# Performance work log

Measured on AMD Instinct MI355X. Metric: run time of the kernel, lower is better.

## Reference

```python
import jax, jax.numpy as jnp
import numpy as np

COEF_DIM = 256  # must match init_kwargs coef_dim


def setup_inputs() -> dict:
    key = jax.random.key(0)
    k1, k2 = jax.random.split(key)
    # times in [0,1); with curr_t=1, t_scaled = 2*t - 1 lies in [-1,1)
    t = jax.random.uniform(k1, (4, 131072), dtype=jnp.float32)
    # learned HiPPO coefficients (buffer `coef` in the torch module)
    coef = jax.random.normal(k2, (COEF_DIM,), dtype=jnp.float32)
    return {"t": t, "coef": coef, "curr_t": 1}


def reference(t, coef, curr_t):
    """Signal reconstruction: sum_{i=1..N} coef[i-1]*sqrt(2i+1)*P_i(2t/curr_t-1).

    Instead of N independent legendre_polynomial_p calls (O(N^2) work),
    run the three-term Legendre recurrence once with lax.scan, fusing the
    coef-weighted accumulation into the carry (O(N) work per time point).
    """
    x = 2.0 * t / curr_t - 1.0            # scaled times, same shape as t
    n = coef.shape[0]
    i = jnp.arange(1, n + 1, dtype=jnp.float32)
    w = coef * jnp.sqrt(2.0 * i + 1.0)    # per-degree weight, degree i=1..N

    def step(carry, wi):
        pm1, p, acc = carry               # P_{deg-1}, P_deg, running sum
        w_next, deg = wi                  # weight for degree deg+1
        # P_{deg+1} = ((2*deg+1)*x*P_deg - deg*P_{deg-1}) / (deg+1)
        p_next = ((2.0 * deg + 1.0) * x * p - deg * pm1) / (deg + 1.0)
        return (p, p_next, acc + w_next * p_next), None

    # P_0 = 1, P_1 = x; accumulator starts with the degree-1 term w[0]*P_1
    init = (jnp.ones_like(x), x, w[0] * x)
    degs = jnp.arange(1, n, dtype=jnp.float32)
    (_, _, out), _ = jax.lax.scan(step, init, (w[1:], degs))
    return out
```

## Files before the change

### kernel.cpp

```cpp
#include <hip/hip_runtime.h>


#define NCOEF 256

__global__ __launch_bounds__(256) void hippo_kernel(
    const float* __restrict__ t,
    const float* __restrict__ coef,
    const int* __restrict__ curr_t,
    float* __restrict__ out,
    int n4)
{
    __shared__ float w[NCOEF];
    const int tid = threadIdx.x;
    w[tid] = coef[tid] * sqrtf(2.0f * (float)tid + 3.0f);
    __syncthreads();

    const int gid = blockIdx.x * 256 + tid;
    if (gid >= n4) return;

    const float s = 2.0f / (float)curr_t[0];

    float4 tv = reinterpret_cast<const float4*>(t)[gid];
    float x[4] = { tv.x * s - 1.0f, tv.y * s - 1.0f,
                   tv.z * s - 1.0f, tv.w * s - 1.0f };

    float pm1[4], p[4], acc[4];
    const float w0 = w[0];
#pragma unroll
    for (int e = 0; e < 4; ++e) {
        pm1[e] = 1.0f;
        p[e]   = x[e];
        acc[e] = w0 * x[e];
    }

#pragma unroll
    for (int d = 1; d < NCOEF; ++d) {
        const float a = (2.0f * (float)d + 1.0f) / ((float)d + 1.0f);
        const float b = (float)d / ((float)d + 1.0f);
        const float wd = w[d];
#pragma unroll
        for (int e = 0; e < 4; ++e) {
            float pn = a * (x[e] * p[e]) - b * pm1[e];
            pm1[e] = p[e];
            p[e]   = pn;
            acc[e] = fmaf(wd, pn, acc[e]);
        }
    }

    reinterpret_cast<float4*>(out)[gid] =
        make_float4(acc[0], acc[1], acc[2], acc[3]);
}

extern "C" void kernel_launch(void* const* d_in, const int* in_sizes, int n_in,
                              void* d_out, int out_size, void* d_ws, size_t ws_size,
                              hipStream_t stream)
{
    const float* t      = (const float*)d_in[0];
    const float* coef   = (const float*)d_in[1];
    const int*   curr_t = (const int*)d_in[2];
    float*       out    = (float*)d_out;

    int n  = in_sizes[0];
    int n4 = n >> 2;
    int blocks = (n4 + 255) / 256;
    hippo_kernel<<<blocks, 256, 0, stream>>>(t, coef, curr_t, out, n4);
}
```

Baseline: 67.23 us.

## Rescale Legendre recurrence to cut per-degree multiplies and pack coefficients in float4 table

Rewrites the Legendre three-term recurrence in a rescaled form, S = P/g with g computed via lgamma, so each step takes one multiply plus one fma instead of a multiply, multiply and fma. Precomputed per-degree constants and rescaled weights go into a shared float4 table, read two degrees per load. The loop is only partly unrolled now (unroll 2) instead of fully unrolled. The rescaling factors come from lgamma/exp, which may change numerical accuracy, and the setup cost per block rises because of the transcendental calls.

```diff
diff --git a/kernel.cpp b/kernel.cpp
--- a/kernel.cpp
+++ b/kernel.cpp
@@ -1,7 +1,20 @@
 #include <hip/hip_runtime.h>
+#include <math.h>
 
 
-#define NCOEF 256
+#define NPAIR 128
+
+__device__ inline float g_of(float fi) {
+    float lg = lgammaf(2.0f * fi) - (fi - 1.0f) * 1.3862943611f
+             - lgammaf(fi) - lgammaf(fi + 1.0f);
+    return expf(lg);
+}
+
+__device__ inline float wp_of(int i, const float* __restrict__ coef) {
+    if (i > 256) return 0.0f;
+    float fi = (float)i;
+    return coef[i - 1] * sqrtf(2.0f * fi + 1.0f) * g_of(fi);
+}
 
 __global__ __launch_bounds__(256) void hippo_kernel(
     const float* __restrict__ t,
@@ -10,9 +23,22 @@
     float* __restrict__ out,
     int n4)
 {
-    __shared__ float w[NCOEF];
+    __shared__ float4 tab[NPAIR + 1];
     const int tid = threadIdx.x;
-    w[tid] = coef[tid] * sqrtf(2.0f * (float)tid + 3.0f);
+
+    if (tid <= NPAIR) {
+        if (tid < NPAIR) {
+            const float d1 = 2.0f * (float)tid + 1.0f;
+            const float d2 = d1 + 1.0f;
+            const float b1 = 4.0f * d1 * d1 / (4.0f * d1 * d1 - 1.0f);
+            const float b2 = 4.0f * d2 * d2 / (4.0f * d2 * d2 - 1.0f);
+            const float w1 = wp_of(2 * tid + 2, coef);
+            const float w2 = wp_of(2 * tid + 3, coef);
+            tab[tid] = make_float4(b1, w1, b2, w2);
+        } else {
+            tab[NPAIR] = make_float4(0.0f, 0.0f, 0.0f, 0.0f);
+        }
+    }
     __syncthreads();
 
     const int gid = blockIdx.x * 256 + tid;
@@ -24,27 +50,32 @@
     float x[4] = { tv.x * s - 1.0f, tv.y * s - 1.0f,
                    tv.z * s - 1.0f, tv.w * s - 1.0f };
 
-    float pm1[4], p[4], acc[4];
-    const float w0 = w[0];
+    const float wp1 = coef[0] * 1.7320508075688772f;
+    float X[4], S[4], Sm1[4], acc[4];
 #pragma unroll
     for (int e = 0; e < 4; ++e) {
-        pm1[e] = 1.0f;
-        p[e]   = x[e];
-        acc[e] = w0 * x[e];
+        X[e]   = 2.0f * x[e];
+        S[e]   = x[e];
+        Sm1[e] = 0.5f;
+        acc[e] = wp1 * x[e];
     }
 
-#pragma unroll
-    for (int d = 1; d < NCOEF; ++d) {
-        const float a = (2.0f * (float)d + 1.0f) / ((float)d + 1.0f);
-        const float b = (float)d / ((float)d + 1.0f);
-        const float wd = w[d];
+    float4 c = tab[0];
+#pragma unroll 2
+    for (int m = 0; m < NPAIR; ++m) {
+        float4 cn = tab[m + 1];
 #pragma unroll
         for (int e = 0; e < 4; ++e) {
-            float pn = a * (x[e] * p[e]) - b * pm1[e];
-            pm1[e] = p[e];
-            p[e]   = pn;
-            acc[e] = fmaf(wd, pn, acc[e]);
+            float t1  = c.x * Sm1[e];
+            float sn1 = fmaf(X[e], S[e], -t1);
+            acc[e] = fmaf(c.y, sn1, acc[e]);
+            float t2  = c.z * S[e];
+            float sn2 = fmaf(X[e], sn1, -t2);
+            acc[e] = fmaf(c.w, sn2, acc[e]);
+            Sm1[e] = sn1;
+            S[e]   = sn2;
         }
+        c = cn;
     }
 
     reinterpret_cast<float4*>(out)[gid] =
```

After: 68.22 us. No clear change (+1.5%).

## Rescale Legendre recurrence to cut per-degree ops and precompute coefficient table

Applied to the files above, without the earlier changes.

The kernel now runs a rescaled Legendre recurrence, S_{n+1} = 2x*S_n - b_n*S_{n-1}. This needs one multiply and two FMAs per degree instead of the earlier mul/mul/fma/fma sequence. A separate single-block kernel builds a pair-unrolled float4 table of recurrence constants and rescaled weights in workspace. The main kernel reads that table through wave-uniform scalar loads and processes one element per thread instead of four. In exchange it adds a second kernel launch and uses an asymptotic series for the scaling factors, which may cost some accuracy at high degree. It also gives up the per-thread ILP that four independent chains provided.

```diff
diff --git a/kernel.cpp b/kernel.cpp
--- a/kernel.cpp
+++ b/kernel.cpp
@@ -1,54 +1,79 @@
 #include <hip/hip_runtime.h>
 
 
-#define NCOEF 256
+#define NPAIR 128
 
-__global__ __launch_bounds__(256) void hippo_kernel(
+__device__ __forceinline__ float g_of(int i) {
+    const float fi = (float)i;
+    float r = 2.0f * rsqrtf(3.14159265358979f * fi);
+    float inv = 1.0f / fi;
+    float corr = 1.0f + inv * (-0.125f + inv * (0.0078125f + inv * 0.0048828125f));
+    float g = r * corr;
+    if (i < 8) {
+        const float gtab[8] = {2.0f, 1.0f, 0.75f, 0.625f, 0.546875f,
+                               0.4921875f, 0.451171875f, 0.4189453125f};
+        g = gtab[i];
+    }
+    return g;
+}
+
+__device__ __forceinline__ float wp_of(int i, const float* __restrict__ coef) {
+    if (i > 256) return 0.0f;
+    float fi = (float)i;
+    return coef[i - 1] * sqrtf(2.0f * fi + 3.0f - 2.0f) * g_of(i);
+}
+
+__global__ __launch_bounds__(256) void build_tab(
+    const float* __restrict__ coef, float4* __restrict__ tab)
+{
+    const int m = threadIdx.x;
+    if (m < NPAIR) {
+        const float d1 = 2.0f * (float)m + 1.0f;
+        const float d2 = d1 + 1.0f;
+        const float b1 = 4.0f * d1 * d1 / (4.0f * d1 * d1 - 1.0f);
+        const float b2 = 4.0f * d2 * d2 / (4.0f * d2 * d2 - 1.0f);
+        tab[m] = make_float4(b1, wp_of(2 * m + 2, coef),
+                             b2, wp_of(2 * m + 3, coef));
+    } else if (m == NPAIR) {
+        tab[NPAIR] = make_float4(0.0f, 0.0f, 0.0f, 0.0f);
+    }
+}
+
+__global__ __launch_bounds__(256, 8) void hippo_main(
     const float* __restrict__ t,
     const float* __restrict__ coef,
     const int* __restrict__ curr_t,
+    const float4* __restrict__ tab,
     float* __restrict__ out,
-    int n4)
+    int n)
 {
-    __shared__ float w[NCOEF];
-    const int tid = threadIdx.x;
-    w[tid] = coef[tid] * sqrtf(2.0f * (float)tid + 3.0f);
-    __syncthreads();
-
-    const int gid = blockIdx.x * 256 + tid;
-    if (gid >= n4) return;
+    const int gid = blockIdx.x * 256 + threadIdx.x;
+    if (gid >= n) return;
 
     const float s = 2.0f / (float)curr_t[0];
+    const float x = fmaf(t[gid], s, -1.0f);
+    const float X = 2.0f * x;
 
-    float4 tv = reinterpret_cast<const float4*>(t)[gid];
-    float x[4] = { tv.x * s - 1.0f, tv.y * s - 1.0f,
-                   tv.z * s - 1.0f, tv.w * s - 1.0f };
+    float Sm1 = 0.5f;
+    float S   = x;
+    float acc = (coef[0] * 1.7320508075688772f) * x;
 
-    float pm1[4], p[4], acc[4];
-    const float w0 = w[0];
-#pragma unroll
-    for (int e = 0; e < 4; ++e) {
-        pm1[e] = 1.0f;
-        p[e]   = x[e];
-        acc[e] = w0 * x[e];
+    float4 c = tab[__builtin_amdgcn_readfirstlane(0)];
+#pragma unroll 2
+    for (int m = 0; m < NPAIR; ++m) {
+        float4 cn = tab[__builtin_amdgcn_readfirstlane(m + 1)];
+        float t1  = c.x * Sm1;
+        float sn1 = fmaf(X, S, -t1);
+        acc = fmaf(c.y, sn1, acc);
+        float t2  = c.z * S;
+        float sn2 = fmaf(X, sn1, -t2);
+        acc = fmaf(c.w, sn2, acc);
+        Sm1 = sn1;
+        S   = sn2;
+        c   = cn;
     }
 
-#pragma unroll
-    for (int d = 1; d < NCOEF; ++d) {
-        const float a = (2.0f * (float)d + 1.0f) / ((float)d + 1.0f);
-        const float b = (float)d / ((float)d + 1.0f);
-        const float wd = w[d];
-#pragma unroll
-        for (int e = 0; e < 4; ++e) {
-            float pn = a * (x[e] * p[e]) - b * pm1[e];
-            pm1[e] = p[e];
-            p[e]   = pn;
-            acc[e] = fmaf(wd, pn, acc[e]);
-        }
-    }
-
-    reinterpret_cast<float4*>(out)[gid] =
-        make_float4(acc[0], acc[1], acc[2], acc[3]);
+    out[gid] = acc;
 }
 
 extern "C" void kernel_launch(void* const* d_in, const int* in_sizes, int n_in,
@@ -59,9 +84,10 @@
     const float* coef   = (const float*)d_in[1];
     const int*   curr_t = (const int*)d_in[2];
     float*       out    = (float*)d_out;
+    float4*      tab    = (float4*)d_ws;
 
-    int n  = in_sizes[0];
-    int n4 = n >> 2;
-    int blocks = (n4 + 255) / 256;
-    hippo_kernel<<<blocks, 256, 0, stream>>>(t, coef, curr_t, out, n4);
+    int n = in_sizes[0];
+    build_tab<<<1, 256, 0, stream>>>(coef, tab);
+    int blocks = (n + 255) / 256;
+    hippo_main<<<blocks, 256, 0, stream>>>(t, coef, curr_t, tab, out, n);
 }
```

Result: slower. 77.30 us (+15.0%).

## Fold sqrt weights into normalized Legendre recurrence and use one element per thread

Applied to the files above, without the earlier changes.

Rescales the recurrence to normalized polynomials q_i = sqrt(2i+1)·P_i and folds the sqrt factors into compile-time constants A and B. The per-degree weight then becomes the raw coef, so the shared-memory weight table and its barrier go away. Coef is read directly from global memory, which is uniform per degree and likely becomes scalar loads. Each thread now handles one element instead of four, giving 4x more threads, less ILP per thread, and 8 blocks per CU as the launch bound.

```diff
diff --git a/kernel.cpp b/kernel.cpp
--- a/kernel.cpp
+++ b/kernel.cpp
@@ -1,54 +1,56 @@
 #include <hip/hip_runtime.h>
 
 
-#define NCOEF 256
+constexpr double csqrt(double v) {
+    double r = v > 1.0 ? v : 1.0;
+    for (int i = 0; i < 64; ++i) r = 0.5 * (r + v / r);
+    return r;
+}
 
-__global__ __launch_bounds__(256) void hippo_kernel(
+template <int I>
+struct Step {
+    static __device__ __forceinline__ void run(const float x, float& qm1,
+                                               float& q, float& acc,
+                                               const float* __restrict__ coef) {
+        constexpr float A = (float)((2.0 * I + 1.0) * csqrt(2.0 * I + 3.0) /
+                                    ((I + 1.0) * csqrt(2.0 * I + 1.0)));
+        constexpr float B = (float)((double)I * csqrt(2.0 * I + 3.0) /
+                                    ((I + 1.0) * csqrt(2.0 * I - 1.0)));
+        float u  = A * q;
+        float v  = B * qm1;
+        float qn = fmaf(x, u, -v);
+        acc = fmaf(coef[I], qn, acc);
+        qm1 = q;
+        q   = qn;
+        Step<I + 1>::run(x, qm1, q, acc, coef);
+    }
+};
+template <>
+struct Step<256> {
+    static __device__ __forceinline__ void run(float, float&, float&, float&,
+                                               const float*) {}
+};
+
+__global__ __launch_bounds__(256, 8) void hippo_kernel(
     const float* __restrict__ t,
     const float* __restrict__ coef,
     const int* __restrict__ curr_t,
     float* __restrict__ out,
-    int n4)
+    int n)
 {
-    __shared__ float w[NCOEF];
-    const int tid = threadIdx.x;
-    w[tid] = coef[tid] * sqrtf(2.0f * (float)tid + 3.0f);
-    __syncthreads();
-
-    const int gid = blockIdx.x * 256 + tid;
-    if (gid >= n4) return;
+    const int gid = blockIdx.x * 256 + threadIdx.x;
+    if (gid >= n) return;
 
     const float s = 2.0f / (float)curr_t[0];
+    const float x = fmaf(t[gid], s, -1.0f);
 
-    float4 tv = reinterpret_cast<const float4*>(t)[gid];
-    float x[4] = { tv.x * s - 1.0f, tv.y * s - 1.0f,
-                   tv.z * s - 1.0f, tv.w * s - 1.0f };
+    float qm1 = 1.0f;
+    float q   = 1.7320508075688772f * x;
+    float acc = coef[0] * q;
 
-    float pm1[4], p[4], acc[4];
-    const float w0 = w[0];
-#pragma unroll
-    for (int e = 0; e < 4; ++e) {
-        pm1[e] = 1.0f;
-        p[e]   = x[e];
-        acc[e] = w0 * x[e];
-    }
+    Step<1>::run(x, qm1, q, acc, coef);
 
-#pragma unroll
-    for (int d = 1; d < NCOEF; ++d) {
-        const float a = (2.0f * (float)d + 1.0f) / ((float)d + 1.0f);
-        const float b = (float)d / ((float)d + 1.0f);
-        const float wd = w[d];
-#pragma unroll
-        for (int e = 0; e < 4; ++e) {
-            float pn = a * (x[e] * p[e]) - b * pm1[e];
-            pm1[e] = p[e];
-            p[e]   = pn;
-            acc[e] = fmaf(wd, pn, acc[e]);
-        }
-    }
-
-    reinterpret_cast<float4*>(out)[gid] =
-        make_float4(acc[0], acc[1], acc[2], acc[3]);
+    out[gid] = acc;
 }
 
 extern "C" void kernel_launch(void* const* d_in, const int* in_sizes, int n_in,
@@ -60,8 +62,7 @@
     const int*   curr_t = (const int*)d_in[2];
     float*       out    = (float*)d_out;
 
-    int n  = in_sizes[0];
-    int n4 = n >> 2;
-    int blocks = (n4 + 255) / 256;
-    hippo_kernel<<<blocks, 256, 0, stream>>>(t, coef, curr_t, out, n4);
+    int n = in_sizes[0];
+    int blocks = (n + 255) / 256;
+    hippo_kernel<<<blocks, 256, 0, stream>>>(t, coef, curr_t, out, n);
 }
```

Result: faster. 65.42 us (-2.7%).
